# Performance work log

Hardware: AMD Instinct MI355X
Metric: run time of the kernel (lower is better)

The kernel has to match this reference:

```python
import jax, jax.numpy as jnp
import numpy as np

B, C, H, W = 8, 64, 64, 64
OUT = 256
N_PAIRS = C * (C + 1) // 2          # 2080 upper-triangular (incl diag) products
N_IN = C + N_PAIRS                  # 2144 conv input channels


def setup_inputs() -> dict:
    key = jax.random.key(0)
    k1, k2 = jax.random.split(key)
    x = jax.random.normal(k1, (B, C, H, W), dtype=jnp.float32)
    fc_w = jax.random.normal(k2, (OUT, N_IN), dtype=jnp.float32) * 0.02
    return {"x": x, "fc_w": fc_w}


def reference(x, fc_w):
    # Upper-triangular indices (row-major, incl diagonal) == get_square_indices(C)
    ii, jj = np.triu_indices(x.shape[1])
    # Per-pixel outer product restricted to the needed triangular terms.
    quad = x[:, ii] * x[:, jj]                  # [B, C(C+1)/2, H, W]
    y = jnp.concatenate([x, quad], axis=1)      # [B, C(C+3)/2, H, W]
    # 1x1 conv, bias=False -> pointwise channel GEMM
    return jnp.einsum('bchw,oc->bohw', y, fc_w)
```

## Files before the change

### kernel.cpp

```cpp
#include <hip/hip_runtime.h>
#include <hip/hip_bf16.h>

using u16 = unsigned short;
using u32 = unsigned int;

typedef __attribute__((ext_vector_type(8)))  short s16x8;
typedef __attribute__((ext_vector_type(2)))  float f32x2;
typedef __attribute__((ext_vector_type(16))) float f32x16;
typedef __attribute__((ext_vector_type(4)))  u32   u32x4;

#define NQ 74
#define WG_U16   (NQ * 2 * 4096)
#define RUNPK_OFF (WG_U16 * 2)

__device__ __forceinline__ u16 f2bf_rne(float f) {
    u32 u = __builtin_bit_cast(u32, f);
    u32 r = u + 0x7fffu + ((u >> 16) & 1u);
    return (u16)(r >> 16);
}
__device__ __forceinline__ float bf2f(u16 u) {
    u32 v = ((u32)u) << 16;
    return __builtin_bit_cast(float, v);
}

__device__ __forceinline__ void run_decode(int r, int& i, int& j0) {
    if (r < 8) { i = 64; j0 = r << 3; return; }
    int rr = r - 8;
    int ii = 0;
    while (true) { int cnt = 8 - (ii >> 3); if (rr < cnt) break; rr -= cnt; ++ii; }
    i = ii;
    j0 = ((ii >> 3) << 3) + (rr << 3);
}

__global__ __launch_bounds__(1024)
void pack_w(const float* __restrict__ fcw, u16* __restrict__ wg,
            u32* __restrict__ runpk) {
    __shared__ u16 runs4[4];
    const int q = blockIdx.x >> 3;
    const int t = threadIdx.x;
    if (t < 4) {
        int i, j0; run_decode(q * 4 + t, i, j0);
        runs4[t] = (u16)((i << 8) | j0);
        if ((blockIdx.x & 7) == 0 && t < 2) {
            int ia, ja, ib, jb;
            run_decode(q * 4 + t * 2 + 0, ia, ja);
            run_decode(q * 4 + t * 2 + 1, ib, jb);
            runpk[q * 2 + t] =
                ((u32)ia << 24) | ((u32)ja << 16) | ((u32)ib << 8) | (u32)jb;
        }
    }
    __syncthreads();
    const u32 g  = blockIdx.x * 1024 + t;
    const int e  = g & 7;
    const int l  = (g >> 3) & 63;
    const int ks = (g >> 9) & 1;
    const int ni = (g >> 10) & 3;
    const int nh = (g >> 12) & 1;
    const int kh = l >> 5;
    const u16 ij = runs4[ks * 2 + kh];
    const int i = ij >> 8, j0 = ij & 255;
    const int n = nh * 128 + ni * 32 + (l & 31);
    const int j = j0 + e;
    float w;
    if (i == 64)    w = fcw[n * 2144 + j];
    else if (j < i) w = 0.f;
    else            w = fcw[n * 2144 + 64 + i * 64 - ((i * (i - 1)) >> 1) + (j - i)];
    wg[g] = f2bf_rne(w);
}

__device__ __forceinline__ s16x8 packmul(float fi, s16x8 vj) {
    u32 pk[4];
    #pragma unroll
    for (int d = 0; d < 4; ++d) {
        float p0 = fi * bf2f((u16)vj[2 * d]);
        float p1 = fi * bf2f((u16)vj[2 * d + 1]);
        pk[d] = __builtin_amdgcn_perm(__builtin_bit_cast(u32, p1),
                                      __builtin_bit_cast(u32, p0), 0x07060302u);
    }
    u32x4 pv = { pk[0], pk[1], pk[2], pk[3] };
    return __builtin_bit_cast(s16x8, pv);
}

__global__ __launch_bounds__(512, 4)
void quad_gemm(const float* __restrict__ x, const u16* __restrict__ wg,
               const u32* __restrict__ runpk, float* __restrict__ out) {
    __shared__ __align__(16) u16 x_lds[128 * 64];
    __shared__ __align__(16) u16 wbuf[3][4096];
    __shared__ u32 runl[NQ * 2];

    const int t   = threadIdx.x;
    const int l   = t & 63;
    const int wv  = t >> 6;
    const int mrow = wv >> 1;
    const int nc   = wv & 1;
    const int kh  = l >> 5;
    const int lm  = l & 31;
    const int sw8 = (lm & 7) << 3;

    const int mtile = blockIdx.x >> 1;
    const int nb    = blockIdx.x & 1;
    const int pix0  = mtile * 128;
    const int b     = pix0 >> 12;
    const int hw0   = pix0 & 4095;

    if (t < NQ * 2) runl[t] = runpk[t];

    {
        const int mg = (t & 63) << 1;
        const int cg = (t >> 6) << 3;
        const float* xp = x + ((size_t)b << 18) + hw0 + mg;
        f32x2 vv[8];
        #pragma unroll
        for (int e = 0; e < 8; ++e)
            vv[e] = *(const f32x2*)(xp + ((size_t)(cg + e) << 12));
        #pragma unroll
        for (int r = 0; r < 2; ++r) {
            int m = mg + r;
            s16x8 pv = { (short)f2bf_rne(vv[0][r]), (short)f2bf_rne(vv[1][r]),
                         (short)f2bf_rne(vv[2][r]), (short)f2bf_rne(vv[3][r]),
                         (short)f2bf_rne(vv[4][r]), (short)f2bf_rne(vv[5][r]),
                         (short)f2bf_rne(vv[6][r]), (short)f2bf_rne(vv[7][r]) };
            *(s16x8*)(x_lds + (m << 6) + (cg ^ ((m & 7) << 3))) = pv;
        }
    }

    const u16* wsrc = wg + (size_t)nb * 4096 + t * 8;
    char* wb0 = (char*)&wbuf[0][0];
    char* wb1 = (char*)&wbuf[1][0];
    char* wb2 = (char*)&wbuf[2][0];
    #define STAGEQ(Q, DST) __builtin_amdgcn_global_load_lds(                  \
        (const __attribute__((address_space(1))) void*)(wsrc + (size_t)(Q) * 8192), \
        (__attribute__((address_space(3))) void*)((DST) + t * 16), 16, 0, 0)
    STAGEQ(0, wb0);
    STAGEQ(1, wb1);

    const int xrow = (mrow * 32 + lm) << 6;

    f32x16 acc0, acc1;
    #pragma unroll
    for (int r = 0; r < 16; ++r) { acc0[r] = 0.f; acc1[r] = 0.f; }

    #define GENQ(Q, Y0_, Y1_) do {                                           \
        u32 rp0_ = runl[(Q) * 2], rp1_ = runl[(Q) * 2 + 1];                  \
        u32 ij0_ = kh ? (rp0_ & 0xffffu) : (rp0_ >> 16);                     \
        u32 ij1_ = kh ? (rp1_ & 0xffffu) : (rp1_ >> 16);                     \
        int ia_ = (int)(ij0_ >> 8), ja_ = (int)(ij0_ & 255u) ^ sw8;          \
        int ib_ = (int)(ij1_ >> 8), jb_ = (int)(ij1_ & 255u) ^ sw8;          \
        float fa_ = (ia_ >= 64) ? 1.0f : bf2f(x_lds[xrow + ((ia_ & 63) ^ sw8)]); \
        float fb_ = (ib_ >= 64) ? 1.0f : bf2f(x_lds[xrow + ((ib_ & 63) ^ sw8)]); \
        Y0_ = packmul(fa_, *(const s16x8*)(x_lds + xrow + ja_));             \
        Y1_ = packmul(fb_, *(const s16x8*)(x_lds + xrow + jb_));             \
    } while (0)

    #define STEP(Q, YC0, YC1, YN0, YN1, LAST) do {                           \
        if (LAST) { asm volatile("s_waitcnt vmcnt(0)" ::: "memory"); }       \
        else      { asm volatile("s_waitcnt vmcnt(1)" ::: "memory"); }       \
        __builtin_amdgcn_s_barrier();                                        \
        asm volatile("" ::: "memory");                                       \
        if ((Q) + 2 < NQ) STAGEQ((Q) + 2, wb2);                              \
        const s16x8* wbp_ = (const s16x8*)wb0;                               \
        s16x8 W00_ = wbp_[(nc * 4 + 0) * 64 + l];                            \
        s16x8 W01_ = wbp_[(nc * 4 + 1) * 64 + l];                            \
        s16x8 W10_ = wbp_[(nc * 4 + 2) * 64 + l];                            \
        s16x8 W11_ = wbp_[(nc * 4 + 3) * 64 + l];                            \
        if (!(LAST)) GENQ((Q) + 1, YN0, YN1);                                \
        acc0 = __builtin_amdgcn_mfma_f32_32x32x16_bf16(W00_, YC0, acc0, 0, 0, 0); \
        acc0 = __builtin_amdgcn_mfma_f32_32x32x16_bf16(W01_, YC1, acc0, 0, 0, 0); \
        acc1 = __builtin_amdgcn_mfma_f32_32x32x16_bf16(W10_, YC0, acc1, 0, 0, 0); \
        acc1 = __builtin_amdgcn_mfma_f32_32x32x16_bf16(W11_, YC1, acc1, 0, 0, 0); \
        char* tp_ = wb0; wb0 = wb1; wb1 = wb2; wb2 = tp_;                    \
    } while (0)

    __syncthreads();

    s16x8 Ya0, Ya1, Yb0, Yb1;
    GENQ(0, Ya0, Ya1);
    for (int q = 0; q < NQ - 2; q += 2) {
        STEP(q,     Ya0, Ya1, Yb0, Yb1, false);
        STEP(q + 1, Yb0, Yb1, Ya0, Ya1, false);
    }
    STEP(NQ - 2, Ya0, Ya1, Yb0, Yb1, false);
    STEP(NQ - 1, Yb0, Yb1, Ya0, Ya1, true);

    float* ob = out + ((size_t)b << 20) + (size_t)hw0;
    const int px = mrow * 32 + lm;
    #pragma unroll
    for (int r = 0; r < 16; ++r) {
        const int o = nb * 128 + nc * 64 + kh * 4 + (r & 3) + 8 * (r >> 2);
        ob[(size_t)o * 4096 + px]        = acc0[r];
        ob[(size_t)(o + 32) * 4096 + px] = acc1[r];
    }
}

extern "C" void kernel_launch(void* const* d_in, const int* in_sizes, int n_in,
                              void* d_out, int out_size, void* d_ws, size_t ws_size,
                              hipStream_t stream) {
    const float* x   = (const float*)d_in[0];
    const float* fcw = (const float*)d_in[1];
    float* out = (float*)d_out;
    u16* wg    = (u16*)d_ws;
    u32* runpk = (u32*)((char*)d_ws + RUNPK_OFF);

    hipLaunchKernelGGL(pack_w, dim3(WG_U16 / 1024), dim3(1024), 0, stream,
                       fcw, wg, runpk);
    hipLaunchKernelGGL(quad_gemm, dim3(512), dim3(512), 0, stream,
                       x, wg, runpk, out);
}
```

Baseline: 129.0 us.

## Use 2x2 register tiles per wave, direct global weight loads, reuse x_j across pairs

Shrinks each block to 4 waves, and each wave now computes a 64x64 output tile with four accumulators instead of two. Weights are loaded straight from global memory into registers with double buffering, replacing the LDS staging and per-step barriers. The triangular pair ordering is reorganised so one x_j vector is multiplied by several x_i scalars, reusing the loaded vector and cutting LDS reads. The trade is more register pressure, fewer waves per block, and weight loads that no longer share LDS reuse across waves.

```diff
diff --git a/kernel.cpp b/kernel.cpp
--- a/kernel.cpp
+++ b/kernel.cpp
@@ -1,16 +1,16 @@
 #include <hip/hip_runtime.h>
-#include <hip/hip_bf16.h>
 
 using u16 = unsigned short;
 using u32 = unsigned int;
 
 typedef __attribute__((ext_vector_type(8)))  short s16x8;
-typedef __attribute__((ext_vector_type(2)))  float f32x2;
+typedef __attribute__((ext_vector_type(4)))  float f32x4;
 typedef __attribute__((ext_vector_type(16))) float f32x16;
 typedef __attribute__((ext_vector_type(4)))  u32   u32x4;
 
-#define NQ 74
-#define WG_U16   (NQ * 2 * 4096)
+#define NQ  74
+#define NQQ 72
+#define WG_U16   (NQ * 8192)
 #define RUNPK_OFF (WG_U16 * 2)
 
 __device__ __forceinline__ u16 f2bf_rne(float f) {
@@ -23,43 +23,32 @@
     return __builtin_bit_cast(float, v);
 }
 
-__device__ __forceinline__ void run_decode(int r, int& i, int& j0) {
-    if (r < 8) { i = 64; j0 = r << 3; return; }
-    int rr = r - 8;
-    int ii = 0;
-    while (true) { int cnt = 8 - (ii >> 3); if (rr < cnt) break; rr -= cnt; ++ii; }
-    i = ii;
-    j0 = ((ii >> 3) << 3) + (rr << 3);
+__device__ __forceinline__ void cm_decode(int r, int& i, int& j0) {
+    if (r >= 288) { i = 64; j0 = (r - 288) * 8; return; }
+    int c = r >> 2;
+    int jr = 0;
+    while (jr < 7 && (jr + 1) * (jr + 2) <= c) ++jr;
+    i  = 4 * (c - jr * (jr + 1)) + (r & 3);
+    j0 = 8 * jr;
 }
 
 __global__ __launch_bounds__(1024)
 void pack_w(const float* __restrict__ fcw, u16* __restrict__ wg,
             u32* __restrict__ runpk) {
-    __shared__ u16 runs4[4];
-    const int q = blockIdx.x >> 3;
-    const int t = threadIdx.x;
-    if (t < 4) {
-        int i, j0; run_decode(q * 4 + t, i, j0);
-        runs4[t] = (u16)((i << 8) | j0);
-        if ((blockIdx.x & 7) == 0 && t < 2) {
-            int ia, ja, ib, jb;
-            run_decode(q * 4 + t * 2 + 0, ia, ja);
-            run_decode(q * 4 + t * 2 + 1, ib, jb);
-            runpk[q * 2 + t] =
-                ((u32)ia << 24) | ((u32)ja << 16) | ((u32)ib << 8) | (u32)jb;
-        }
-    }
-    __syncthreads();
-    const u32 g  = blockIdx.x * 1024 + t;
+    const u32 g = blockIdx.x * 1024 + threadIdx.x;
+    if (blockIdx.x == 0 && threadIdx.x < NQQ) {
+        int q = threadIdx.x, jr = 0;
+        while (jr < 7 && (jr + 1) * (jr + 2) <= q) ++jr;
+        runpk[q] = ((u32)(8 * jr) << 8) | (u32)(4 * (q - jr * (jr + 1)));
+    }
     const int e  = g & 7;
     const int l  = (g >> 3) & 63;
-    const int ks = (g >> 9) & 1;
-    const int ni = (g >> 10) & 3;
-    const int nh = (g >> 12) & 1;
     const int kh = l >> 5;
-    const u16 ij = runs4[ks * 2 + kh];
-    const int i = ij >> 8, j0 = ij & 255;
-    const int n = nh * 128 + ni * 32 + (l & 31);
+    const int ni = (g >> 9) & 1, s = (g >> 10) & 1;
+    const int nc = (g >> 11) & 1, nb = (g >> 12) & 1;
+    const int q  = g >> 13;
+    int i, j0; cm_decode(q * 4 + 2 * s + kh, i, j0);
+    const int n = nb * 128 + nc * 64 + ni * 32 + (l & 31);
     const int j = j0 + e;
     float w;
     if (i == 64)    w = fcw[n * 2144 + j];
@@ -81,114 +70,136 @@
     return __builtin_bit_cast(s16x8, pv);
 }
 
-__global__ __launch_bounds__(512, 4)
+__global__ __launch_bounds__(256, 2)
 void quad_gemm(const float* __restrict__ x, const u16* __restrict__ wg,
                const u32* __restrict__ runpk, float* __restrict__ out) {
-    __shared__ __align__(16) u16 x_lds[128 * 64];
-    __shared__ __align__(16) u16 wbuf[3][4096];
-    __shared__ u32 runl[NQ * 2];
-
-    const int t   = threadIdx.x;
-    const int l   = t & 63;
-    const int wv  = t >> 6;
-    const int mrow = wv >> 1;
-    const int nc   = wv & 1;
-    const int kh  = l >> 5;
-    const int lm  = l & 31;
-    const int sw8 = (lm & 7) << 3;
-
-    const int mtile = blockIdx.x >> 1;
+    __shared__ __align__(16) u16 xl[128 * 64];
+
+    const int t  = threadIdx.x;
+    const int l  = t & 63;
+    const int wv = t >> 6;
+    const int mrow = wv >> 1, nc = wv & 1;
+    const int lm = l & 31, kh = l >> 5;
+    const int sw = (lm & 7) << 3;
+
+    const int mtile = (int)blockIdx.x >> 1;
     const int nb    = blockIdx.x & 1;
     const int pix0  = mtile * 128;
     const int b     = pix0 >> 12;
     const int hw0   = pix0 & 4095;
 
-    if (t < NQ * 2) runl[t] = runpk[t];
-
     {
-        const int mg = (t & 63) << 1;
-        const int cg = (t >> 6) << 3;
-        const float* xp = x + ((size_t)b << 18) + hw0 + mg;
-        f32x2 vv[8];
+        const int mg = (t & 31) * 4;
+        const int cg = (t >> 5) * 8;
+        const float* xp = x + ((size_t)b << 18) + (size_t)cg * 4096 + hw0 + mg;
+        f32x4 vv[8];
         #pragma unroll
         for (int e = 0; e < 8; ++e)
-            vv[e] = *(const f32x2*)(xp + ((size_t)(cg + e) << 12));
-        #pragma unroll
-        for (int r = 0; r < 2; ++r) {
+            vv[e] = *(const f32x4*)(xp + (size_t)e * 4096);
+        #pragma unroll
+        for (int r = 0; r < 4; ++r) {
+            u32 w4[4];
+            #pragma unroll
+            for (int d = 0; d < 4; ++d)
+                w4[d] = (u32)f2bf_rne(vv[2 * d][r]) |
+                        ((u32)f2bf_rne(vv[2 * d + 1][r]) << 16);
             int m = mg + r;
-            s16x8 pv = { (short)f2bf_rne(vv[0][r]), (short)f2bf_rne(vv[1][r]),
-                         (short)f2bf_rne(vv[2][r]), (short)f2bf_rne(vv[3][r]),
-                         (short)f2bf_rne(vv[4][r]), (short)f2bf_rne(vv[5][r]),
-                         (short)f2bf_rne(vv[6][r]), (short)f2bf_rne(vv[7][r]) };
-            *(s16x8*)(x_lds + (m << 6) + (cg ^ ((m & 7) << 3))) = pv;
+            u32x4 pv = { w4[0], w4[1], w4[2], w4[3] };
+            *(u32x4*)(xl + m * 64 + (cg ^ ((m & 7) << 3))) = pv;
         }
     }
 
-    const u16* wsrc = wg + (size_t)nb * 4096 + t * 8;
-    char* wb0 = (char*)&wbuf[0][0];
-    char* wb1 = (char*)&wbuf[1][0];
-    char* wb2 = (char*)&wbuf[2][0];
-    #define STAGEQ(Q, DST) __builtin_amdgcn_global_load_lds(                  \
-        (const __attribute__((address_space(1))) void*)(wsrc + (size_t)(Q) * 8192), \
-        (__attribute__((address_space(3))) void*)((DST) + t * 16), 16, 0, 0)
-    STAGEQ(0, wb0);
-    STAGEQ(1, wb1);
-
-    const int xrow = (mrow * 32 + lm) << 6;
-
-    f32x16 acc0, acc1;
+    const int pxb = mrow * 64 + lm;
+    const u16* wp = wg + (size_t)(nb * 2 + nc) * 2048 + (size_t)l * 8;
+
+    f32x16 acc[2][2];
     #pragma unroll
-    for (int r = 0; r < 16; ++r) { acc0[r] = 0.f; acc1[r] = 0.f; }
-
-    #define GENQ(Q, Y0_, Y1_) do {                                           \
-        u32 rp0_ = runl[(Q) * 2], rp1_ = runl[(Q) * 2 + 1];                  \
-        u32 ij0_ = kh ? (rp0_ & 0xffffu) : (rp0_ >> 16);                     \
-        u32 ij1_ = kh ? (rp1_ & 0xffffu) : (rp1_ >> 16);                     \
-        int ia_ = (int)(ij0_ >> 8), ja_ = (int)(ij0_ & 255u) ^ sw8;          \
-        int ib_ = (int)(ij1_ >> 8), jb_ = (int)(ij1_ & 255u) ^ sw8;          \
-        float fa_ = (ia_ >= 64) ? 1.0f : bf2f(x_lds[xrow + ((ia_ & 63) ^ sw8)]); \
-        float fb_ = (ib_ >= 64) ? 1.0f : bf2f(x_lds[xrow + ((ib_ & 63) ^ sw8)]); \
-        Y0_ = packmul(fa_, *(const s16x8*)(x_lds + xrow + ja_));             \
-        Y1_ = packmul(fb_, *(const s16x8*)(x_lds + xrow + jb_));             \
+    for (int mi = 0; mi < 2; ++mi)
+        #pragma unroll
+        for (int ni = 0; ni < 2; ++ni)
+            #pragma unroll
+            for (int r = 0; r < 16; ++r) acc[mi][ni][r] = 0.f;
+
+    #define LOADW(Q, W) do {                                                 \
+        const u32x4* p_ = (const u32x4*)(wp + (size_t)(Q) * 8192);           \
+        W[0] = p_[0]; W[1] = p_[64]; W[2] = p_[128]; W[3] = p_[192];         \
     } while (0)
 
-    #define STEP(Q, YC0, YC1, YN0, YN1, LAST) do {                           \
-        if (LAST) { asm volatile("s_waitcnt vmcnt(0)" ::: "memory"); }       \
-        else      { asm volatile("s_waitcnt vmcnt(1)" ::: "memory"); }       \
-        __builtin_amdgcn_s_barrier();                                        \
-        asm volatile("" ::: "memory");                                       \
-        if ((Q) + 2 < NQ) STAGEQ((Q) + 2, wb2);                              \
-        const s16x8* wbp_ = (const s16x8*)wb0;                               \
-        s16x8 W00_ = wbp_[(nc * 4 + 0) * 64 + l];                            \
-        s16x8 W01_ = wbp_[(nc * 4 + 1) * 64 + l];                            \
-        s16x8 W10_ = wbp_[(nc * 4 + 2) * 64 + l];                            \
-        s16x8 W11_ = wbp_[(nc * 4 + 3) * 64 + l];                            \
-        if (!(LAST)) GENQ((Q) + 1, YN0, YN1);                                \
-        acc0 = __builtin_amdgcn_mfma_f32_32x32x16_bf16(W00_, YC0, acc0, 0, 0, 0); \
-        acc0 = __builtin_amdgcn_mfma_f32_32x32x16_bf16(W01_, YC1, acc0, 0, 0, 0); \
-        acc1 = __builtin_amdgcn_mfma_f32_32x32x16_bf16(W10_, YC0, acc1, 0, 0, 0); \
-        acc1 = __builtin_amdgcn_mfma_f32_32x32x16_bf16(W11_, YC1, acc1, 0, 0, 0); \
-        char* tp_ = wb0; wb0 = wb1; wb1 = wb2; wb2 = tp_;                    \
+    #define GENQ(Q, Y) do {                                                  \
+        if ((Q) < NQQ) {                                                     \
+            u32 meta_ = runpk[(Q)];                                          \
+            int j0_ = (int)((meta_ >> 8) & 255u), ib_ = (int)(meta_ & 255u); \
+            _Pragma("unroll")                                                \
+            for (int mi_ = 0; mi_ < 2; ++mi_) {                              \
+                int base_ = (pxb + mi_ * 32) * 64;                           \
+                s16x8 vj_ = *(const s16x8*)(xl + base_ + (j0_ ^ sw));        \
+                float f0_ = bf2f(xl[base_ + ((ib_ + kh) ^ sw)]);             \
+                float f1_ = bf2f(xl[base_ + ((ib_ + 2 + kh) ^ sw)]);         \
+                Y[mi_ * 2 + 0] = packmul(f0_, vj_);                          \
+                Y[mi_ * 2 + 1] = packmul(f1_, vj_);                          \
+            }                                                                \
+        } else {                                                             \
+            int cb_ = ((Q) - NQQ) * 32;                                      \
+            _Pragma("unroll")                                                \
+            for (int mi_ = 0; mi_ < 2; ++mi_) {                              \
+                int base_ = (pxb + mi_ * 32) * 64;                           \
+                _Pragma("unroll")                                            \
+                for (int s_ = 0; s_ < 2; ++s_) {                             \
+                    int j0_ = cb_ + 8 * (2 * s_ + kh);                       \
+                    Y[mi_ * 2 + s_] =                                        \
+                        *(const s16x8*)(xl + base_ + (j0_ ^ sw));            \
+                }                                                            \
+            }                                                                \
+        }                                                                    \
     } while (0)
 
+    #define MFMAQ(W, Y) do {                                                 \
+        _Pragma("unroll")                                                    \
+        for (int s_ = 0; s_ < 2; ++s_)                                       \
+            _Pragma("unroll")                                                \
+            for (int mi_ = 0; mi_ < 2; ++mi_)                                \
+                _Pragma("unroll")                                            \
+                for (int ni_ = 0; ni_ < 2; ++ni_)                            \
+                    acc[mi_][ni_] = __builtin_amdgcn_mfma_f32_32x32x16_bf16( \
+                        __builtin_bit_cast(s16x8, W[s_ * 2 + ni_]),          \
+                        Y[mi_ * 2 + s_],                                     \
+                        acc[mi_][ni_], 0, 0, 0);                             \
+    } while (0)
+
+    u32x4 Wa[4], Wb[4];
+    s16x8 Ya[4], Yb[4];
+
+    LOADW(0, Wa);
     __syncthreads();
-
-    s16x8 Ya0, Ya1, Yb0, Yb1;
-    GENQ(0, Ya0, Ya1);
-    for (int q = 0; q < NQ - 2; q += 2) {
-        STEP(q,     Ya0, Ya1, Yb0, Yb1, false);
-        STEP(q + 1, Yb0, Yb1, Ya0, Ya1, false);
-    }
-    STEP(NQ - 2, Ya0, Ya1, Yb0, Yb1, false);
-    STEP(NQ - 1, Yb0, Yb1, Ya0, Ya1, true);
+    GENQ(0, Ya);
+
+    #pragma unroll 1
+    for (int q = 0; q + 2 < NQ; q += 2) {
+        LOADW(q + 1, Wb);
+        GENQ(q + 1, Yb);
+        MFMAQ(Wa, Ya);
+        LOADW(q + 2, Wa);
+        GENQ(q + 2, Ya);
+        MFMAQ(Wb, Yb);
+    }
+    LOADW(NQ - 1, Wb);
+    GENQ(NQ - 1, Yb);
+    MFMAQ(Wa, Ya);
+    MFMAQ(Wb, Yb);
 
     float* ob = out + ((size_t)b << 20) + (size_t)hw0;
-    const int px = mrow * 32 + lm;
     #pragma unroll
-    for (int r = 0; r < 16; ++r) {
-        const int o = nb * 128 + nc * 64 + kh * 4 + (r & 3) + 8 * (r >> 2);
-        ob[(size_t)o * 4096 + px]        = acc0[r];
-        ob[(size_t)(o + 32) * 4096 + px] = acc1[r];
+    for (int mi = 0; mi < 2; ++mi) {
+        const int px = pxb + mi * 32;
+        #pragma unroll
+        for (int ni = 0; ni < 2; ++ni) {
+            #pragma unroll
+            for (int r = 0; r < 16; ++r) {
+                const int o = nb * 128 + nc * 64 + ni * 32 +
+                              (r & 3) + 8 * (r >> 2) + 4 * kh;
+                ob[(size_t)o * 4096 + px] = acc[mi][ni][r];
+            }
+        }
     }
 }
 
@@ -203,6 +214,6 @@
 
     hipLaunchKernelGGL(pack_w, dim3(WG_U16 / 1024), dim3(1024), 0, stream,
                        fcw, wg, runpk);
-    hipLaunchKernelGGL(quad_gemm, dim3(512), dim3(512), 0, stream,
+    hipLaunchKernelGGL(quad_gemm, dim3(512), dim3(256), 0, stream,
                        x, wg, runpk, out);
 }
```

Result: faster. 114.7 us (-11.1%).
